# Kernel optimization log

Hardware: AMD Instinct MI355X
Metric: run time of the kernel (lower is better)

## Reference

```python
import jax, jax.numpy as jnp
import numpy as np

N_NODES = 50000
N_EDGES = 800000
D_IN, D_HID, D_LAT = 128, 128, 64
BN_EPS = 1e-5


def setup_inputs() -> dict:
    key = jax.random.key(0)
    ks = jax.random.split(key, 8)
    x = jax.random.normal(ks[0], (N_NODES, D_IN), dtype=jnp.float32)
    edge_index = jax.random.randint(ks[1], (2, N_EDGES), 0, N_NODES, dtype=jnp.int64)
    s1 = 1.0 / np.sqrt(D_IN)
    s2 = 1.0 / np.sqrt(D_HID)
    W1 = jax.random.normal(ks[2], (D_IN, D_HID), dtype=jnp.float32) * s1
    b1 = jnp.zeros((D_HID,), jnp.float32)
    gamma = jnp.ones((D_HID,), jnp.float32)
    beta = jnp.zeros((D_HID,), jnp.float32)
    Wmu = jax.random.normal(ks[3], (D_HID, D_LAT), dtype=jnp.float32) * s2
    bmu = jnp.zeros((D_LAT,), jnp.float32)
    Wls = jax.random.normal(ks[4], (D_HID, D_LAT), dtype=jnp.float32) * s2
    bls = jnp.zeros((D_LAT,), jnp.float32)
    return {"x": x, "edge_index": edge_index, "W1": W1, "b1": b1,
            "gamma": gamma, "beta": beta, "Wmu": Wmu, "bmu": bmu,
            "Wls": Wls, "bls": bls}


def _gcn_conv(h, src, dst, norm_e, inv_deg, W, b):
    # PyG GCNConv: linear transform, then sym-normalized aggregation (A+I).
    h = h @ W                                   # [N, F]
    msgs = h[src] * norm_e[:, None]             # gather + edge scaling, [E, F]
    agg = jax.ops.segment_sum(msgs, dst, num_segments=h.shape[0])
    # self-loop contribution: norm[i]*norm[i] = 1/deg[i]
    return agg + h * inv_deg[:, None] + b


def reference(x, edge_index, W1, b1, gamma, beta, Wmu, bmu, Wls, bls):
    src, dst = edge_index[0], edge_index[1]
    n = x.shape[0]
    # degrees including self loops (GCN symmetric normalization)
    deg = jax.ops.segment_sum(jnp.ones(dst.shape, x.dtype), dst, num_segments=n) + 1.0
    inv_sqrt_deg = jax.lax.rsqrt(deg)
    norm_e = inv_sqrt_deg[src] * inv_sqrt_deg[dst]   # per-edge norm, [E]
    inv_deg = 1.0 / deg

    h = _gcn_conv(x, src, dst, norm_e, inv_deg, W1, b1)
    # BatchNorm1d with batch statistics (biased var), then ReLU; dropout off (eval)
    mean = h.mean(axis=0)
    var = h.var(axis=0)
    h = (h - mean) * jax.lax.rsqrt(var + BN_EPS) * gamma + beta
    h = jax.nn.relu(h)

    mu = _gcn_conv(h, src, dst, norm_e, inv_deg, Wmu, bmu)
    log_std = _gcn_conv(h, src, dst, norm_e, inv_deg, Wls, bls)
    return mu, log_std
```

## Files before the change

### kernel.cpp

```cpp
#include <hip/hip_runtime.h>
#include <hip/hip_bf16.h>

#define N_NODES 50000
#define N_EDGES 800000
#define F 128
#define L 64
#define BN_EPS 1e-5f
#define SCAN_BLOCKS 196
#define BN_BLOCKS 391
#define NPART 8
#define PART_SZ 6250
#define FILL_BLOCKS 2048

typedef __attribute__((ext_vector_type(8))) short short8;
typedef __attribute__((ext_vector_type(8))) unsigned short ushort8;
typedef __attribute__((ext_vector_type(4))) float f32x4;

static __device__ __forceinline__ float loadF(const void* p, int i, int f32) {
    if (f32) return ((const float*)p)[i];
    return __bfloat162float(((const __hip_bfloat16*)p)[i]);
}
static __device__ __forceinline__ int loadI(const void* p, int i, int i64) {
    if (i64) return (int)((const long long*)p)[i];
    return ((const int*)p)[i];
}
static __device__ __forceinline__ float bfu2f(unsigned short u) {
    unsigned int t = ((unsigned int)u) << 16;
    float f;
    __builtin_memcpy(&f, &t, 4);
    return f;
}
static __device__ __forceinline__ short f2bf_s(float f) {
    union { __hip_bfloat16 b; short s; } cv;
    cv.b = __float2bfloat16(f);
    return cv.s;
}
static __device__ __forceinline__ unsigned short f2bf_u(float f) {
    union { __hip_bfloat16 b; unsigned short u; } cv;
    cv.b = __float2bfloat16(f);
    return cv.u;
}

__global__ void k_prep(const void* __restrict__ W1, const void* __restrict__ Wmu,
                       const void* __restrict__ Wls, const unsigned short* __restrict__ xs,
                       const int* __restrict__ ei, __hip_bfloat16* __restrict__ Wt1,
                       __hip_bfloat16* __restrict__ Wt2, int* __restrict__ flags,
                       int* __restrict__ degi) {
    int b = blockIdx.x;
    int t = threadIdx.x;
    if (b == 0) {
        __shared__ int cnt[2];
        if (t < 2) cnt[t] = 0;
        __syncthreads();
        unsigned short v = xs[2 * t];
        int e = (v >> 7) & 0xff;
        int sane = (e >= 112 && e <= 133) ? 1 : 0;
        if (v == 0 || v == 0x8000) sane = 1;
        atomicAdd(&cnt[0], sane);
        atomicAdd(&cnt[1], (ei[2 * t + 1] != 0) ? 1 : 0);
        __syncthreads();
        if (t == 0) {
            flags[0] = (cnt[0] < 128) ? 1 : 0;
            flags[1] = (cnt[1] < 8) ? 1 : 0;
        }
    } else if (b <= 64) {
        __shared__ int cnt;
        if (t == 0) cnt = 0;
        __syncthreads();
        unsigned short v = ((const unsigned short*)W1)[2 * t];
        int e = (v >> 7) & 0xff;
        atomicAdd(&cnt, (e >= 100 && e <= 133) ? 1 : 0);
        __syncthreads();
        int f32 = (cnt < 128) ? 1 : 0;
        int idx = (b - 1) * 256 + t;
        int n = idx >> 7, k = idx & 127;
        Wt1[idx] = __float2bfloat16(loadF(W1, k * F + n, f32));
        float v2 = (n < L) ? loadF(Wmu, k * L + n, f32) : loadF(Wls, k * L + (n - L), f32);
        Wt2[idx] = __float2bfloat16(v2);
    } else {
        int i = (b - 65) * 256 + t;
        if (i < N_NODES) degi[i] = 0;
    }
}

__global__ void k_eiprep(const void* ei, const int* __restrict__ flags,
                         int* __restrict__ src32, int* __restrict__ dst32,
                         int* __restrict__ degi) {
    int e = blockIdx.x * blockDim.x + threadIdx.x;
    if (e < N_EDGES) {
        int i64 = flags[1];
        int d = loadI(ei, N_EDGES + e, i64);
        if (i64) {
            src32[e] = loadI(ei, e, 1);
            dst32[e] = d;
        }
        atomicAdd(&degi[d], 1);
    }
}

__global__ void k_bsum(const int* __restrict__ degi, int* __restrict__ bsum) {
    int i = blockIdx.x * 256 + threadIdx.x;
    int v = (i < N_NODES) ? degi[i] : 0;
#pragma unroll
    for (int o = 32; o; o >>= 1) v += __shfl_down(v, o);
    __shared__ int ws[4];
    if ((threadIdx.x & 63) == 0) ws[threadIdx.x >> 6] = v;
    __syncthreads();
    if (threadIdx.x == 0) bsum[blockIdx.x] = ws[0] + ws[1] + ws[2] + ws[3];
}

__global__ void k_scanb(const int* __restrict__ bsum, int* __restrict__ boff,
                        int* __restrict__ offs) {
    __shared__ int s[256];
    int t = threadIdx.x;
    int v = (t < SCAN_BLOCKS) ? bsum[t] : 0;
    s[t] = v;
    __syncthreads();
    for (int o = 1; o < 256; o <<= 1) {
        int u = (t >= o) ? s[t - o] : 0;
        __syncthreads();
        s[t] += u;
        __syncthreads();
    }
    boff[t] = s[t] - v;
    if (t == 0) offs[N_NODES] = N_EDGES;
}

__global__ void k_offs(int* __restrict__ degi, const int* __restrict__ boff,
                       int* __restrict__ offs, float* __restrict__ isd) {
    __shared__ int s[256];
    int i = blockIdx.x * 256 + threadIdx.x;
    int t = threadIdx.x;
    int v = (i < N_NODES) ? degi[i] : 0;
    s[t] = v;
    __syncthreads();
    for (int o = 1; o < 256; o <<= 1) {
        int u = (t >= o) ? s[t - o] : 0;
        __syncthreads();
        s[t] += u;
        __syncthreads();
    }
    if (i < N_NODES) {
        offs[i] = boff[blockIdx.x] + s[t] - v;
        isd[i] = 1.0f / sqrtf((float)v + 1.0f);
        degi[i] = 0;
    }
}

__global__ void k_fill(const int* __restrict__ ei32, const int* __restrict__ src32,
                       const int* __restrict__ dst32, const int* __restrict__ flags,
                       const int* __restrict__ offs, int* __restrict__ cur,
                       int* __restrict__ csr) {
    const int* sp;
    const int* dp;
    if (flags[1]) { sp = src32; dp = dst32; }
    else          { sp = ei32;  dp = ei32 + N_EDGES; }
    int grp = blockIdx.x & (NPART - 1);
    int sub = blockIdx.x >> 3;
    int lo = grp * PART_SZ, hi = lo + PART_SZ;
    int stride = (FILL_BLOCKS >> 3) * 256;
    for (int e = sub * 256 + threadIdx.x; e < N_EDGES; e += stride) {
        int d = dp[e];
        if (d >= lo && d < hi) {
            int pos = offs[d] + atomicAdd(&cur[d], 1);
            csr[pos] = sp[e];
        }
    }
}

__global__ __launch_bounds__(256) void k_gemm_mfma(const void* __restrict__ Xin,
        const __hip_bfloat16* __restrict__ Wt, const float* __restrict__ isd,
        const int* __restrict__ flags, int mode,
        const float* __restrict__ bnscale, const float* __restrict__ bnshift,
        unsigned short* __restrict__ outb) {
    int wave = threadIdx.x >> 6, lane = threadIdx.x & 63;
    int quad = lane >> 4, mr = lane & 15;
    int m0 = blockIdx.x * 64 + wave * 16;
    int row = m0 + mr;
    if (row >= N_NODES) row = N_NODES - 1;
    short8 a[4];
    if (mode == 1) {
        const unsigned short* xb = (const unsigned short*)Xin;
#pragma unroll
        for (int t = 0; t < 4; ++t) {
            int k0 = t * 32 + quad * 8;
            ushort8 raw = *(const ushort8*)(xb + row * F + k0);
            short8 av;
#pragma unroll
            for (int j = 0; j < 8; ++j) {
                float v = bfu2f(raw[j]) * bnscale[k0 + j] + bnshift[k0 + j];
                av[j] = f2bf_s(fmaxf(v, 0.f));
            }
            a[t] = av;
        }
    } else if (flags[0]) {
        const float* xf = (const float*)Xin;
#pragma unroll
        for (int t = 0; t < 4; ++t) {
            int off = row * F + t * 32 + quad * 8;
            short8 av;
#pragma unroll
            for (int j = 0; j < 8; ++j) av[j] = f2bf_s(xf[off + j]);
            a[t] = av;
        }
    } else {
        const short* xb = (const short*)Xin;
#pragma unroll
        for (int t = 0; t < 4; ++t)
            a[t] = *(const short8*)(xb + row * F + t * 32 + quad * 8);
    }
    f32x4 acc[8];
    const short* wb = (const short*)Wt;
#pragma unroll
    for (int nt = 0; nt < 8; ++nt) {
        const short* wp = wb + (nt * 16 + mr) * F + quad * 8;
        f32x4 c = {0.f, 0.f, 0.f, 0.f};
        c = __builtin_amdgcn_mfma_f32_16x16x32_bf16(a[0], *(const short8*)(wp), c, 0, 0, 0);
        c = __builtin_amdgcn_mfma_f32_16x16x32_bf16(a[1], *(const short8*)(wp + 32), c, 0, 0, 0);
        c = __builtin_amdgcn_mfma_f32_16x16x32_bf16(a[2], *(const short8*)(wp + 64), c, 0, 0, 0);
        c = __builtin_amdgcn_mfma_f32_16x16x32_bf16(a[3], *(const short8*)(wp + 96), c, 0, 0, 0);
        acc[nt] = c;
    }
    float sd[4];
    int orow[4];
#pragma unroll
    for (int r = 0; r < 4; ++r) {
        orow[r] = m0 + quad * 4 + r;
        sd[r] = (orow[r] < N_NODES) ? isd[orow[r]] : 0.f;
    }
#pragma unroll
    for (int nt = 0; nt < 8; ++nt)
#pragma unroll
        for (int r = 0; r < 4; ++r)
            if (orow[r] < N_NODES)
                outb[orow[r] * F + nt * 16 + mr] = f2bf_u(acc[nt][r] * sd[r]);
}

__global__ void k_agg1(const unsigned short* __restrict__ val, const int* __restrict__ csr,
                       const int* __restrict__ offs, const float* __restrict__ isd,
                       const void* __restrict__ b1, const int* __restrict__ flags,
                       unsigned short* __restrict__ out) {
    int node = blockIdx.x * 4 + (threadIdx.x >> 6);
    if (node >= N_NODES) return;
    int lane = threadIdx.x & 63;
    int grp = lane >> 4, l16 = lane & 15;
    const ushort8* vp = (const ushort8*)val;
    float acc[8] = {0.f, 0.f, 0.f, 0.f, 0.f, 0.f, 0.f, 0.f};
    if (grp == 0) {
        ushort8 u = vp[node * 16 + l16];
#pragma unroll
        for (int j = 0; j < 8; ++j) acc[j] = bfu2f(u[j]);
    }
    int end = offs[node + 1];
    int i = offs[node] + grp;
    for (; i + 4 < end; i += 8) {
        ushort8 u0 = vp[csr[i] * 16 + l16];
        ushort8 u1 = vp[csr[i + 4] * 16 + l16];
#pragma unroll
        for (int j = 0; j < 8; ++j) acc[j] += bfu2f(u0[j]) + bfu2f(u1[j]);
    }
    for (; i < end; i += 4) {
        ushort8 u = vp[csr[i] * 16 + l16];
#pragma unroll
        for (int j = 0; j < 8; ++j) acc[j] += bfu2f(u[j]);
    }
#pragma unroll
    for (int j = 0; j < 8; ++j) {
        acc[j] += __shfl_xor(acc[j], 16);
        acc[j] += __shfl_xor(acc[j], 32);
    }
    if (grp == 0) {
        float sd = isd[node];
        int c0 = l16 * 8, f32 = flags[0];
        ushort8 r;
#pragma unroll
        for (int j = 0; j < 8; ++j) r[j] = f2bf_u(acc[j] * sd + loadF(b1, c0 + j, f32));
        ((ushort8*)out)[node * 16 + l16] = r;
    }
}

__global__ void k_bnstats(const unsigned short* __restrict__ h, float* __restrict__ partial) {
    __shared__ float ls[256][8];
    __shared__ float lq[256][8];
    int t = threadIdx.x;
    int o = t & 15, rg = t >> 4;
    int row0 = blockIdx.x * 128 + rg;
    float s[8] = {0.f}, q[8] = {0.f};
#pragma unroll
    for (int i = 0; i < 8; ++i) {
        int row = row0 + i * 16;
        if (row < N_NODES) {
            ushort8 u = *(const ushort8*)(h + row * F + o * 8);
#pragma unroll
            for (int j = 0; j < 8; ++j) {
                float v = bfu2f(u[j]);
                s[j] += v;
                q[j] += v * v;
            }
        }
    }
#pragma unroll
    for (int j = 0; j < 8; ++j) { ls[t][j] = s[j]; lq[t][j] = q[j]; }
    __syncthreads();
    if (t < 128) {
        int c = t, oo = c >> 3, jj = c & 7;
        float ts = 0.f, tq = 0.f;
#pragma unroll
        for (int rgi = 0; rgi < 16; ++rgi) {
            ts += ls[rgi * 16 + oo][jj];
            tq += lq[rgi * 16 + oo][jj];
        }
        partial[blockIdx.x * 256 + c] = ts;
        partial[blockIdx.x * 256 + 128 + c] = tq;
    }
}

__global__ void k_bnredprep(const float* __restrict__ partial, const void* __restrict__ gamma,
                            const void* __restrict__ beta, const int* __restrict__ flags,
                            float* __restrict__ scale, float* __restrict__ shift) {
    int c = blockIdx.x;
    float s = 0.f, q = 0.f;
    for (int b = threadIdx.x; b < BN_BLOCKS; b += 256) {
        s += partial[b * 256 + c];
        q += partial[b * 256 + 128 + c];
    }
#pragma unroll
    for (int o = 32; o; o >>= 1) {
        s += __shfl_down(s, o);
        q += __shfl_down(q, o);
    }
    __shared__ float ws[4], wq[4];
    if ((threadIdx.x & 63) == 0) {
        ws[threadIdx.x >> 6] = s;
        wq[threadIdx.x >> 6] = q;
    }
    __syncthreads();
    if (threadIdx.x == 0) {
        float S = ws[0] + ws[1] + ws[2] + ws[3];
        float Q = wq[0] + wq[1] + wq[2] + wq[3];
        const float invN = 1.0f / (float)N_NODES;
        float m = S * invN;
        float var = Q * invN - m * m;
        int f32 = flags[0];
        float sc = loadF(gamma, c, f32) * rsqrtf(var + BN_EPS);
        scale[c] = sc;
        shift[c] = loadF(beta, c, f32) - m * sc;
    }
}

__global__ void k_agg2(const unsigned short* __restrict__ val, const int* __restrict__ csr,
                       const int* __restrict__ offs, const float* __restrict__ isd,
                       const void* __restrict__ bmu, const void* __restrict__ bls,
                       const int* __restrict__ flags, void* __restrict__ out) {
    int node = blockIdx.x * 4 + (threadIdx.x >> 6);
    if (node >= N_NODES) return;
    int lane = threadIdx.x & 63;
    int grp = lane >> 4, l16 = lane & 15;
    const ushort8* vp = (const ushort8*)val;
    float acc[8] = {0.f, 0.f, 0.f, 0.f, 0.f, 0.f, 0.f, 0.f};
    if (grp == 0) {
        ushort8 u = vp[node * 16 + l16];
#pragma unroll
        for (int j = 0; j < 8; ++j) acc[j] = bfu2f(u[j]);
    }
    int end = offs[node + 1];
    int i = offs[node] + grp;
    for (; i + 4 < end; i += 8) {
        ushort8 u0 = vp[csr[i] * 16 + l16];
        ushort8 u1 = vp[csr[i + 4] * 16 + l16];
#pragma unroll
        for (int j = 0; j < 8; ++j) acc[j] += bfu2f(u0[j]) + bfu2f(u1[j]);
    }
    for (; i < end; i += 4) {
        ushort8 u = vp[csr[i] * 16 + l16];
#pragma unroll
        for (int j = 0; j < 8; ++j) acc[j] += bfu2f(u[j]);
    }
#pragma unroll
    for (int j = 0; j < 8; ++j) {
        acc[j] += __shfl_xor(acc[j], 16);
        acc[j] += __shfl_xor(acc[j], 32);
    }
    if (grp == 0) {
        float sd = isd[node];
        int c0 = l16 * 8, f32 = flags[0];
        int hsel = (c0 >= L) ? 1 : 0;
        int cc = c0 - hsel * L;
        const void* bp = hsel ? bls : bmu;
        float o8[8];
#pragma unroll
        for (int j = 0; j < 8; ++j) o8[j] = acc[j] * sd + loadF(bp, cc + j, f32);
        long base_o = (long)hsel * (N_NODES * 64) + (long)node * 64 + cc;
        if (f32) {
            float4 r0 = make_float4(o8[0], o8[1], o8[2], o8[3]);
            float4 r1 = make_float4(o8[4], o8[5], o8[6], o8[7]);
            *(float4*)((float*)out + base_o) = r0;
            *(float4*)((float*)out + base_o + 4) = r1;
        } else {
            ushort8 r;
#pragma unroll
            for (int j = 0; j < 8; ++j) r[j] = f2bf_u(o8[j]);
            *(ushort8*)((__hip_bfloat16*)out + base_o) = r;
        }
    }
}

extern "C" void kernel_launch(void* const* d_in, const int* in_sizes, int n_in,
                              void* d_out, int out_size, void* d_ws, size_t ws_size,
                              hipStream_t stream) {
    const void* x     = d_in[0];
    const void* ei    = d_in[1];
    const void* W1    = d_in[2];
    const void* b1    = d_in[3];
    const void* gamma = d_in[4];
    const void* beta  = d_in[5];
    const void* Wmu   = d_in[6];
    const void* bmu   = d_in[7];
    const void* Wls   = d_in[8];
    const void* bls   = d_in[9];

    int*   degi  = (int*)d_ws;
    int*   offs  = degi + 50048;
    float* isd   = (float*)(offs + 50048);
    float* stats = isd + 50000;
    int*   flags = (int*)(stats + 512);
    int*   bsum  = flags + 16;
    int*   boff  = bsum + 256;
    int*   csr   = boff + 256;
    int*   src32 = csr + 800000;
    int*   dst32 = src32 + 800000;
    __hip_bfloat16* Wt1 = (__hip_bfloat16*)(dst32 + 800000);
    __hip_bfloat16* Wt2 = Wt1 + 16384;
    unsigned short* Abf = (unsigned short*)(Wt2 + 16384);
    unsigned short* Hpre = Abf + N_NODES * F;
    float* partial = (float*)(Hpre + N_NODES * F);

    const int NT = 256;
    const int AGG_BLOCKS = (N_NODES + 3) / 4;
    const int GEMM_BLOCKS = (N_NODES + 63) / 64;

    k_prep<<<65 + SCAN_BLOCKS, NT, 0, stream>>>(W1, Wmu, Wls, (const unsigned short*)x,
                                                (const int*)ei, Wt1, Wt2, flags, degi);
    k_eiprep<<<(N_EDGES + NT - 1) / NT, NT, 0, stream>>>(ei, flags, src32, dst32, degi);
    k_bsum<<<SCAN_BLOCKS, NT, 0, stream>>>(degi, bsum);
    k_scanb<<<1, NT, 0, stream>>>(bsum, boff, offs);
    k_offs<<<SCAN_BLOCKS, NT, 0, stream>>>(degi, boff, offs, isd);
    k_fill<<<FILL_BLOCKS, NT, 0, stream>>>((const int*)ei, src32, dst32, flags,
                                           offs, degi, csr);

    k_gemm_mfma<<<GEMM_BLOCKS, NT, 0, stream>>>(x, Wt1, isd, flags, 0, nullptr, nullptr, Abf);
    k_agg1<<<AGG_BLOCKS, NT, 0, stream>>>(Abf, csr, offs, isd, b1, flags, Hpre);

    k_bnstats<<<BN_BLOCKS, NT, 0, stream>>>(Hpre, partial);
    k_bnredprep<<<128, NT, 0, stream>>>(partial, gamma, beta, flags, stats, stats + 128);

    k_gemm_mfma<<<GEMM_BLOCKS, NT, 0, stream>>>(Hpre, Wt2, isd, flags, 1,
                                                stats, stats + 128, Abf);
    k_agg2<<<AGG_BLOCKS, NT, 0, stream>>>(Abf, csr, offs, isd, bmu, bls, flags, d_out);
}
```

Measured before the change: 315.4 us.

## Slice node features into 16-column planes for aggregation and fuse scan kernels

Feature matrices are stored as eight column slices of 16 bf16 values per node, and the aggregation kernels run one block per slice per group of four nodes. Each gather then fetches 32 contiguous bytes, which is meant to keep each slice's working set small enough to stay in cache. The three-kernel degree scan is merged into one kernel that uses a last-block ticket and a spin-wait across blocks, saving two launches. The spin-wait relies on all 196 blocks being resident at once, and the aggregation now issues many more small loads per node.

```diff
diff --git a/kernel.cpp b/kernel.cpp
--- a/kernel.cpp
+++ b/kernel.cpp
@@ -11,6 +11,8 @@
 #define NPART 8
 #define PART_SZ 6250
 #define FILL_BLOCKS 2048
+#define SLICE 16
+#define AGG_BLOCKS 100000
 
 typedef __attribute__((ext_vector_type(8))) short short8;
 typedef __attribute__((ext_vector_type(8))) unsigned short ushort8;
@@ -63,6 +65,7 @@
             flags[0] = (cnt[0] < 128) ? 1 : 0;
             flags[1] = (cnt[1] < 8) ? 1 : 0;
         }
+        if (t == 8 || t == 9) flags[t] = 0;
     } else if (b <= 64) {
         __shared__ int cnt;
         if (t == 0) cnt = 0;
@@ -98,39 +101,13 @@
     }
 }
 
-__global__ void k_bsum(const int* __restrict__ degi, int* __restrict__ bsum) {
-    int i = blockIdx.x * 256 + threadIdx.x;
-    int v = (i < N_NODES) ? degi[i] : 0;
-#pragma unroll
-    for (int o = 32; o; o >>= 1) v += __shfl_down(v, o);
-    __shared__ int ws[4];
-    if ((threadIdx.x & 63) == 0) ws[threadIdx.x >> 6] = v;
-    __syncthreads();
-    if (threadIdx.x == 0) bsum[blockIdx.x] = ws[0] + ws[1] + ws[2] + ws[3];
-}
-
-__global__ void k_scanb(const int* __restrict__ bsum, int* __restrict__ boff,
-                        int* __restrict__ offs) {
+__global__ void k_scan(int* __restrict__ degi, int* __restrict__ offs,
+                       float* __restrict__ isd, int* __restrict__ bsum,
+                       int* __restrict__ boff, int* __restrict__ sync) {
     __shared__ int s[256];
-    int t = threadIdx.x;
-    int v = (t < SCAN_BLOCKS) ? bsum[t] : 0;
-    s[t] = v;
-    __syncthreads();
-    for (int o = 1; o < 256; o <<= 1) {
-        int u = (t >= o) ? s[t - o] : 0;
-        __syncthreads();
-        s[t] += u;
-        __syncthreads();
-    }
-    boff[t] = s[t] - v;
-    if (t == 0) offs[N_NODES] = N_EDGES;
-}
-
-__global__ void k_offs(int* __restrict__ degi, const int* __restrict__ boff,
-                       int* __restrict__ offs, float* __restrict__ isd) {
-    __shared__ int s[256];
-    int i = blockIdx.x * 256 + threadIdx.x;
-    int t = threadIdx.x;
+    __shared__ int ticket, baseSh;
+    int b = blockIdx.x, t = threadIdx.x;
+    int i = b * 256 + t;
     int v = (i < N_NODES) ? degi[i] : 0;
     s[t] = v;
     __syncthreads();
@@ -140,11 +117,36 @@
         s[t] += u;
         __syncthreads();
     }
+    int incl = s[t];
+    if (t == 0) atomicExch(&bsum[b], s[255]);
+    if (t == 0) ticket = atomicAdd(&sync[0], 1);
+    __syncthreads();
+    if (ticket == SCAN_BLOCKS - 1) {
+        int bv = (t < SCAN_BLOCKS) ? atomicAdd(&bsum[t], 0) : 0;
+        __syncthreads();
+        s[t] = bv;
+        __syncthreads();
+        for (int o = 1; o < 256; o <<= 1) {
+            int u = (t >= o) ? s[t - o] : 0;
+            __syncthreads();
+            s[t] += u;
+            __syncthreads();
+        }
+        atomicExch(&boff[t], s[t] - bv);
+        __syncthreads();
+        if (t == 0) atomicExch(&sync[1], 1);
+    }
+    if (t == 0) {
+        while (atomicAdd(&sync[1], 0) == 0) {}
+        baseSh = atomicAdd(&boff[b], 0);
+    }
+    __syncthreads();
     if (i < N_NODES) {
-        offs[i] = boff[blockIdx.x] + s[t] - v;
-        isd[i] = 1.0f / sqrtf((float)v + 1.0f);
+        offs[i] = baseSh + incl - v;
+        isd[i] = rsqrtf((float)v + 1.0f);
         degi[i] = 0;
     }
+    if (b == 0 && t == 0) offs[N_NODES] = N_EDGES;
 }
 
 __global__ void k_fill(const int* __restrict__ ei32, const int* __restrict__ src32,
@@ -184,7 +186,8 @@
 #pragma unroll
         for (int t = 0; t < 4; ++t) {
             int k0 = t * 32 + quad * 8;
-            ushort8 raw = *(const ushort8*)(xb + row * F + k0);
+            int sl = t * 2 + (quad >> 1), woff = (quad & 1) * 8;
+            ushort8 raw = *(const ushort8*)(xb + sl * (N_NODES * SLICE) + row * SLICE + woff);
             short8 av;
 #pragma unroll
             for (int j = 0; j < 8; ++j) {
@@ -233,49 +236,46 @@
 #pragma unroll
         for (int r = 0; r < 4; ++r)
             if (orow[r] < N_NODES)
-                outb[orow[r] * F + nt * 16 + mr] = f2bf_u(acc[nt][r] * sd[r]);
+                outb[nt * (N_NODES * SLICE) + orow[r] * SLICE + mr] = f2bf_u(acc[nt][r] * sd[r]);
 }
 
 __global__ void k_agg1(const unsigned short* __restrict__ val, const int* __restrict__ csr,
                        const int* __restrict__ offs, const float* __restrict__ isd,
                        const void* __restrict__ b1, const int* __restrict__ flags,
                        unsigned short* __restrict__ out) {
-    int node = blockIdx.x * 4 + (threadIdx.x >> 6);
-    if (node >= N_NODES) return;
+    int g = blockIdx.x & 7;
+    int node = (blockIdx.x >> 3) * 4 + (threadIdx.x >> 6);
     int lane = threadIdx.x & 63;
-    int grp = lane >> 4, l16 = lane & 15;
-    const ushort8* vp = (const ushort8*)val;
-    float acc[8] = {0.f, 0.f, 0.f, 0.f, 0.f, 0.f, 0.f, 0.f};
-    if (grp == 0) {
-        ushort8 u = vp[node * 16 + l16];
-#pragma unroll
-        for (int j = 0; j < 8; ++j) acc[j] = bfu2f(u[j]);
+    int sub = lane >> 3, c2 = lane & 7;
+    const unsigned short* vs = val + g * (N_NODES * SLICE);
+    float ax = 0.f, ay = 0.f;
+    if (sub == 0) {
+        ushort2 u = *(const ushort2*)(vs + node * SLICE + c2 * 2);
+        ax = bfu2f(u.x); ay = bfu2f(u.y);
     }
     int end = offs[node + 1];
-    int i = offs[node] + grp;
-    for (; i + 4 < end; i += 8) {
-        ushort8 u0 = vp[csr[i] * 16 + l16];
-        ushort8 u1 = vp[csr[i + 4] * 16 + l16];
-#pragma unroll
-        for (int j = 0; j < 8; ++j) acc[j] += bfu2f(u0[j]) + bfu2f(u1[j]);
-    }
-    for (; i < end; i += 4) {
-        ushort8 u = vp[csr[i] * 16 + l16];
-#pragma unroll
-        for (int j = 0; j < 8; ++j) acc[j] += bfu2f(u[j]);
-    }
-#pragma unroll
-    for (int j = 0; j < 8; ++j) {
-        acc[j] += __shfl_xor(acc[j], 16);
-        acc[j] += __shfl_xor(acc[j], 32);
-    }
-    if (grp == 0) {
+    int i = offs[node] + sub;
+    for (; i + 8 < end; i += 16) {
+        int s0 = csr[i], s1 = csr[i + 8];
+        ushort2 u0 = *(const ushort2*)(vs + s0 * SLICE + c2 * 2);
+        ushort2 u1 = *(const ushort2*)(vs + s1 * SLICE + c2 * 2);
+        ax += bfu2f(u0.x) + bfu2f(u1.x);
+        ay += bfu2f(u0.y) + bfu2f(u1.y);
+    }
+    for (; i < end; i += 8) {
+        ushort2 u = *(const ushort2*)(vs + csr[i] * SLICE + c2 * 2);
+        ax += bfu2f(u.x); ay += bfu2f(u.y);
+    }
+    ax += __shfl_xor(ax, 8);  ay += __shfl_xor(ay, 8);
+    ax += __shfl_xor(ax, 16); ay += __shfl_xor(ay, 16);
+    ax += __shfl_xor(ax, 32); ay += __shfl_xor(ay, 32);
+    if (sub == 0) {
         float sd = isd[node];
-        int c0 = l16 * 8, f32 = flags[0];
-        ushort8 r;
-#pragma unroll
-        for (int j = 0; j < 8; ++j) r[j] = f2bf_u(acc[j] * sd + loadF(b1, c0 + j, f32));
-        ((ushort8*)out)[node * 16 + l16] = r;
+        int c = g * SLICE + c2 * 2, f32 = flags[0];
+        ushort2 r;
+        r.x = f2bf_u(ax * sd + loadF(b1, c, f32));
+        r.y = f2bf_u(ay * sd + loadF(b1, c + 1, f32));
+        *(ushort2*)(out + g * (N_NODES * SLICE) + node * SLICE + c2 * 2) = r;
     }
 }
 
@@ -284,13 +284,15 @@
     __shared__ float lq[256][8];
     int t = threadIdx.x;
     int o = t & 15, rg = t >> 4;
+    int sl = o >> 1, woff = (o & 1) * 8;
+    const unsigned short* hs = h + sl * (N_NODES * SLICE);
     int row0 = blockIdx.x * 128 + rg;
     float s[8] = {0.f}, q[8] = {0.f};
 #pragma unroll
     for (int i = 0; i < 8; ++i) {
         int row = row0 + i * 16;
         if (row < N_NODES) {
-            ushort8 u = *(const ushort8*)(h + row * F + o * 8);
+            ushort8 u = *(const ushort8*)(hs + row * SLICE + woff);
 #pragma unroll
             for (int j = 0; j < 8; ++j) {
                 float v = bfu2f(u[j]);
@@ -352,55 +354,49 @@
                        const int* __restrict__ offs, const float* __restrict__ isd,
                        const void* __restrict__ bmu, const void* __restrict__ bls,
                        const int* __restrict__ flags, void* __restrict__ out) {
-    int node = blockIdx.x * 4 + (threadIdx.x >> 6);
-    if (node >= N_NODES) return;
+    int g = blockIdx.x & 7;
+    int node = (blockIdx.x >> 3) * 4 + (threadIdx.x >> 6);
     int lane = threadIdx.x & 63;
-    int grp = lane >> 4, l16 = lane & 15;
-    const ushort8* vp = (const ushort8*)val;
-    float acc[8] = {0.f, 0.f, 0.f, 0.f, 0.f, 0.f, 0.f, 0.f};
-    if (grp == 0) {
-        ushort8 u = vp[node * 16 + l16];
-#pragma unroll
-        for (int j = 0; j < 8; ++j) acc[j] = bfu2f(u[j]);
+    int sub = lane >> 3, c2 = lane & 7;
+    const unsigned short* vs = val + g * (N_NODES * SLICE);
+    float ax = 0.f, ay = 0.f;
+    if (sub == 0) {
+        ushort2 u = *(const ushort2*)(vs + node * SLICE + c2 * 2);
+        ax = bfu2f(u.x); ay = bfu2f(u.y);
     }
     int end = offs[node + 1];
-    int i = offs[node] + grp;
-    for (; i + 4 < end; i += 8) {
-        ushort8 u0 = vp[csr[i] * 16 + l16];
-        ushort8 u1 = vp[csr[i + 4] * 16 + l16];
-#pragma unroll
-        for (int j = 0; j < 8; ++j) acc[j] += bfu2f(u0[j]) + bfu2f(u1[j]);
-    }
-    for (; i < end; i += 4) {
-        ushort8 u = vp[csr[i] * 16 + l16];
-#pragma unroll
-        for (int j = 0; j < 8; ++j) acc[j] += bfu2f(u[j]);
-    }
-#pragma unroll
-    for (int j = 0; j < 8; ++j) {
-        acc[j] += __shfl_xor(acc[j], 16);
-        acc[j] += __shfl_xor(acc[j], 32);
-    }
-    if (grp == 0) {
+    int i = offs[node] + sub;
+    for (; i + 8 < end; i += 16) {
+        int s0 = csr[i], s1 = csr[i + 8];
+        ushort2 u0 = *(const ushort2*)(vs + s0 * SLICE + c2 * 2);
+        ushort2 u1 = *(const ushort2*)(vs + s1 * SLICE + c2 * 2);
+        ax += bfu2f(u0.x) + bfu2f(u1.x);
+        ay += bfu2f(u0.y) + bfu2f(u1.y);
+    }
+    for (; i < end; i += 8) {
+        ushort2 u = *(const ushort2*)(vs + csr[i] * SLICE + c2 * 2);
+        ax += bfu2f(u.x); ay += bfu2f(u.y);
+    }
+    ax += __shfl_xor(ax, 8);  ay += __shfl_xor(ay, 8);
+    ax += __shfl_xor(ax, 16); ay += __shfl_xor(ay, 16);
+    ax += __shfl_xor(ax, 32); ay += __shfl_xor(ay, 32);
+    if (sub == 0) {
         float sd = isd[node];
-        int c0 = l16 * 8, f32 = flags[0];
-        int hsel = (c0 >= L) ? 1 : 0;
-        int cc = c0 - hsel * L;
+        int c = g * SLICE + c2 * 2, f32 = flags[0];
+        int hsel = (g >= 4) ? 1 : 0;
+        int cc = c - hsel * 64;
         const void* bp = hsel ? bls : bmu;
-        float o8[8];
-#pragma unroll
-        for (int j = 0; j < 8; ++j) o8[j] = acc[j] * sd + loadF(bp, cc + j, f32);
+        float o0 = ax * sd + loadF(bp, cc, f32);
+        float o1 = ay * sd + loadF(bp, cc + 1, f32);
         long base_o = (long)hsel * (N_NODES * 64) + (long)node * 64 + cc;
         if (f32) {
-            float4 r0 = make_float4(o8[0], o8[1], o8[2], o8[3]);
-            float4 r1 = make_float4(o8[4], o8[5], o8[6], o8[7]);
-            *(float4*)((float*)out + base_o) = r0;
-            *(float4*)((float*)out + base_o + 4) = r1;
+            float2 r = make_float2(o0, o1);
+            *(float2*)((float*)out + base_o) = r;
         } else {
-            ushort8 r;
-#pragma unroll
-            for (int j = 0; j < 8; ++j) r[j] = f2bf_u(o8[j]);
-            *(ushort8*)((__hip_bfloat16*)out + base_o) = r;
+            ushort2 r;
+            r.x = f2bf_u(o0);
+            r.y = f2bf_u(o1);
+            *(ushort2*)((__hip_bfloat16*)out + base_o) = r;
         }
     }
 }
@@ -436,15 +432,12 @@
     float* partial = (float*)(Hpre + N_NODES * F);
 
     const int NT = 256;
-    const int AGG_BLOCKS = (N_NODES + 3) / 4;
     const int GEMM_BLOCKS = (N_NODES + 63) / 64;
 
     k_prep<<<65 + SCAN_BLOCKS, NT, 0, stream>>>(W1, Wmu, Wls, (const unsigned short*)x,
                                                 (const int*)ei, Wt1, Wt2, flags, degi);
     k_eiprep<<<(N_EDGES + NT - 1) / NT, NT, 0, stream>>>(ei, flags, src32, dst32, degi);
-    k_bsum<<<SCAN_BLOCKS, NT, 0, stream>>>(degi, bsum);
-    k_scanb<<<1, NT, 0, stream>>>(bsum, boff, offs);
-    k_offs<<<SCAN_BLOCKS, NT, 0, stream>>>(degi, boff, offs, isd);
+    k_scan<<<SCAN_BLOCKS, NT, 0, stream>>>(degi, offs, isd, bsum, boff, flags + 8);
     k_fill<<<FILL_BLOCKS, NT, 0, stream>>>((const int*)ei, src32, dst32, flags,
                                            offs, degi, csr);
 
```

Result: slower. 452.2 us (+43.3%).

## Fuse three-kernel degree scan into one kernel with last-block ticket

Applied to the files above, without the earlier changes.

Replaces the separate block-sum, block-offset scan and offset-write kernels with a single kernel. Each block scans locally and publishes its total; the last block to arrive, chosen by an atomic ticket, scans the block totals and raises a flag that the other blocks spin on. This removes two kernel launches and their inter-kernel gaps. It relies on all 196 blocks being co-resident, or the spin-wait can deadlock.

```diff
diff --git a/kernel.cpp b/kernel.cpp
--- a/kernel.cpp
+++ b/kernel.cpp
@@ -63,6 +63,7 @@
             flags[0] = (cnt[0] < 128) ? 1 : 0;
             flags[1] = (cnt[1] < 8) ? 1 : 0;
         }
+        if (t == 8 || t == 9) flags[t] = 0;
     } else if (b <= 64) {
         __shared__ int cnt;
         if (t == 0) cnt = 0;
@@ -98,39 +99,13 @@
     }
 }
 
-__global__ void k_bsum(const int* __restrict__ degi, int* __restrict__ bsum) {
-    int i = blockIdx.x * 256 + threadIdx.x;
-    int v = (i < N_NODES) ? degi[i] : 0;
-#pragma unroll
-    for (int o = 32; o; o >>= 1) v += __shfl_down(v, o);
-    __shared__ int ws[4];
-    if ((threadIdx.x & 63) == 0) ws[threadIdx.x >> 6] = v;
-    __syncthreads();
-    if (threadIdx.x == 0) bsum[blockIdx.x] = ws[0] + ws[1] + ws[2] + ws[3];
-}
-
-__global__ void k_scanb(const int* __restrict__ bsum, int* __restrict__ boff,
-                        int* __restrict__ offs) {
+__global__ void k_scan(int* __restrict__ degi, int* __restrict__ offs,
+                       float* __restrict__ isd, int* __restrict__ bsum,
+                       int* __restrict__ boff, int* __restrict__ sync) {
     __shared__ int s[256];
-    int t = threadIdx.x;
-    int v = (t < SCAN_BLOCKS) ? bsum[t] : 0;
-    s[t] = v;
-    __syncthreads();
-    for (int o = 1; o < 256; o <<= 1) {
-        int u = (t >= o) ? s[t - o] : 0;
-        __syncthreads();
-        s[t] += u;
-        __syncthreads();
-    }
-    boff[t] = s[t] - v;
-    if (t == 0) offs[N_NODES] = N_EDGES;
-}
-
-__global__ void k_offs(int* __restrict__ degi, const int* __restrict__ boff,
-                       int* __restrict__ offs, float* __restrict__ isd) {
-    __shared__ int s[256];
-    int i = blockIdx.x * 256 + threadIdx.x;
-    int t = threadIdx.x;
+    __shared__ int ticket, baseSh;
+    int b = blockIdx.x, t = threadIdx.x;
+    int i = b * 256 + t;
     int v = (i < N_NODES) ? degi[i] : 0;
     s[t] = v;
     __syncthreads();
@@ -140,11 +115,36 @@
         s[t] += u;
         __syncthreads();
     }
+    int incl = s[t];
+    if (t == 0) atomicExch(&bsum[b], s[255]);
+    if (t == 0) ticket = atomicAdd(&sync[0], 1);
+    __syncthreads();
+    if (ticket == SCAN_BLOCKS - 1) {
+        int bv = (t < SCAN_BLOCKS) ? atomicAdd(&bsum[t], 0) : 0;
+        __syncthreads();
+        s[t] = bv;
+        __syncthreads();
+        for (int o = 1; o < 256; o <<= 1) {
+            int u = (t >= o) ? s[t - o] : 0;
+            __syncthreads();
+            s[t] += u;
+            __syncthreads();
+        }
+        atomicExch(&boff[t], s[t] - bv);
+        __syncthreads();
+        if (t == 0) atomicExch(&sync[1], 1);
+    }
+    if (t == 0) {
+        while (atomicAdd(&sync[1], 0) == 0) {}
+        baseSh = atomicAdd(&boff[b], 0);
+    }
+    __syncthreads();
     if (i < N_NODES) {
-        offs[i] = boff[blockIdx.x] + s[t] - v;
-        isd[i] = 1.0f / sqrtf((float)v + 1.0f);
+        offs[i] = baseSh + incl - v;
+        isd[i] = rsqrtf((float)v + 1.0f);
         degi[i] = 0;
     }
+    if (b == 0 && t == 0) offs[N_NODES] = N_EDGES;
 }
 
 __global__ void k_fill(const int* __restrict__ ei32, const int* __restrict__ src32,
@@ -303,15 +303,15 @@
     for (int j = 0; j < 8; ++j) { ls[t][j] = s[j]; lq[t][j] = q[j]; }
     __syncthreads();
     if (t < 128) {
-        int c = t, oo = c >> 3, jj = c & 7;
+        int oo = t >> 3, jj = t & 7;
         float ts = 0.f, tq = 0.f;
 #pragma unroll
         for (int rgi = 0; rgi < 16; ++rgi) {
             ts += ls[rgi * 16 + oo][jj];
             tq += lq[rgi * 16 + oo][jj];
         }
-        partial[blockIdx.x * 256 + c] = ts;
-        partial[blockIdx.x * 256 + 128 + c] = tq;
+        partial[blockIdx.x * 256 + t] = ts;
+        partial[blockIdx.x * 256 + 128 + t] = tq;
     }
 }
 
@@ -442,9 +442,7 @@
     k_prep<<<65 + SCAN_BLOCKS, NT, 0, stream>>>(W1, Wmu, Wls, (const unsigned short*)x,
                                                 (const int*)ei, Wt1, Wt2, flags, degi);
     k_eiprep<<<(N_EDGES + NT - 1) / NT, NT, 0, stream>>>(ei, flags, src32, dst32, degi);
-    k_bsum<<<SCAN_BLOCKS, NT, 0, stream>>>(degi, bsum);
-    k_scanb<<<1, NT, 0, stream>>>(bsum, boff, offs);
-    k_offs<<<SCAN_BLOCKS, NT, 0, stream>>>(degi, boff, offs, isd);
+    k_scan<<<SCAN_BLOCKS, NT, 0, stream>>>(degi, offs, isd, bsum, boff, flags + 8);
     k_fill<<<FILL_BLOCKS, NT, 0, stream>>>((const int*)ei, src32, dst32, flags,
                                            offs, degi, csr);
 
```

New measurement: 317.0 us. No clear change (+0.5%).
